# Kernel optimization log

Hardware: AMD Instinct MI355X
Metric: run time of the kernel (lower is better)

The kernel has to match this reference:

```python
import jax, jax.numpy as jnp
import numpy as np

B, L, D = 64, 512, 256
BT = 4            # behavior_types (== last dim of bs_seq)
USERS = 10000     # user_num
EPS = 1e-8


def _ln(x, w, b):
    u = x.mean(-1, keepdims=True)
    s = ((x - u) ** 2).mean(-1, keepdims=True)
    return w * (x - u) / jnp.sqrt(s + EPS) + b


def setup_inputs() -> dict:
    key = jax.random.key(0)
    ks = jax.random.split(key, 32)
    lin = lambda k: 0.02 * jax.random.normal(k, (D, D), dtype=jnp.float32)
    inp = {
        'u': jax.random.randint(ks[0], (B,), 0, USERS + 1),
        'seq_logits': jax.random.normal(ks[1], (B, L, D), dtype=jnp.float32),
        'item_emb': jax.random.normal(ks[2], (B, L, D), dtype=jnp.float32),
        'pos_emb': jax.random.normal(ks[3], (B, L, D), dtype=jnp.float32),
        'bs_seq': jax.random.randint(ks[4], (B, L, BT), 0, 2, dtype=jnp.int32),
        'bs_emb': jax.random.normal(ks[5], (B, L, D), dtype=jnp.float32),
        'attn_mask': jnp.zeros((B, 1, L, L), dtype=jnp.float32),
        'user_tables': 0.02 * jax.random.normal(ks[6], (USERS + 1, BT + 1), dtype=jnp.float32),
        'Wq_ib': lin(ks[7]), 'bq_ib': jnp.zeros(D),
        'Wk_ib': lin(ks[8]), 'bk_ib': jnp.zeros(D),
        'Wv_ib': lin(ks[9]), 'bv_ib': jnp.zeros(D),
        'Wq_pb': lin(ks[10]), 'bq_pb': jnp.zeros(D),
        'Wk_pb': lin(ks[11]), 'bk_pb': jnp.zeros(D),
        'Wv_pb': lin(ks[12]), 'bv_pb': jnp.zeros(D),
        'Wf': lin(ks[13]), 'bf': jnp.zeros(D),
        'ln_qib_w': jnp.ones(D), 'ln_qib_b': jnp.zeros(D),
        'ln_qpb_w': jnp.ones(D), 'ln_qpb_b': jnp.zeros(D),
        'ln_f_w': jnp.ones(D), 'ln_f_b': jnp.zeros(D),
    }
    return inp


def reference(u, seq_logits, item_emb, pos_emb, bs_seq, bs_emb, attn_mask,
              user_tables, Wq_ib, bq_ib, Wk_ib, bk_ib, Wv_ib, bv_ib,
              Wq_pb, bq_pb, Wk_pb, bk_pb, Wv_pb, bv_pb, Wf, bf,
              ln_qib_w, ln_qib_b, ln_qpb_w, ln_qpb_b, ln_f_w, ln_f_b):
    mask = attn_mask[:, 0]                      # (B, L, L)
    scale = 1.0 / jnp.sqrt(jnp.float32(D))

    # hamming-distance bias: pdist(hamming)*BT == integer mismatch count (bt==BT)
    dist_idx = jnp.sum(bs_seq[:, :, None, :] != bs_seq[:, None, :, :], axis=-1)  # (B,L,L) int
    tab = user_tables[u]                        # (B, BT+1) per-user transition table
    ham = jax.vmap(lambda t, idx: t[idx])(tab, dist_idx) * scale   # (B, L, L)
    ham_probs = jax.nn.softmax(ham + mask, axis=-1)

    def branch(x_in, ln_w, ln_b, Wq, bq, Wk, bk, Wv, bv):
        q = _ln(x_in, ln_w, ln_b) @ Wq + bq
        k = x_in @ Wk + bk
        v = x_in @ Wv + bv
        scores = jnp.einsum('bqd,bkd->bqk', q, k) * scale
        probs = jax.nn.softmax(scores + mask, axis=-1) + ham_probs
        return jnp.einsum('bqk,bkd->bqd', probs, v)

    ib = branch(item_emb + bs_emb, ln_qib_w, ln_qib_b, Wq_ib, bq_ib, Wk_ib, bk_ib, Wv_ib, bv_ib)
    pb = branch(pos_emb + bs_emb, ln_qpb_w, ln_qpb_b, Wq_pb, bq_pb, Wk_pb, bk_pb, Wv_pb, bv_pb)

    mha = (ib + pb) @ Wf + bf
    return _ln(mha + seq_logits + bs_emb, ln_f_w, ln_f_b)
```

## Files before the change

kernel.cpp:

```cpp
#include <hip/hip_runtime.h>
#include <hip/hip_bf16.h>
#include <math.h>

#define TB 256

typedef short bf16x8 __attribute__((ext_vector_type(8)));
typedef float f32x4 __attribute__((ext_vector_type(4)));
typedef unsigned short ushort_t;
typedef unsigned short us4 __attribute__((ext_vector_type(4)));
typedef unsigned short us8 __attribute__((ext_vector_type(8)));

constexpr int Bc = 64, Lc = 512, Dc = 256;
constexpr float kScale = 0.0625f;
constexpr float kEps = 1e-8f;

__device__ __forceinline__ ushort_t f2bf(float x) {
    union { float f; unsigned u; } v; v.f = x;
    unsigned r = v.u + 0x7fffu + ((v.u >> 16) & 1u);
    return (ushort_t)(r >> 16);
}
__device__ __forceinline__ float bf2f(ushort_t h) {
    union { float f; unsigned u; } v; v.u = ((unsigned)h) << 16;
    return v.f;
}
__device__ __forceinline__ void split1(float x, ushort_t& h, ushort_t& l) {
    h = f2bf(x);
    l = f2bf(x - bf2f(h));
}

__device__ __forceinline__ float sel5(float t0, float t1, float t2, float t3, float t4, int i) {
    float r = t0;
    r = (i == 1) ? t1 : r;
    r = (i == 2) ? t2 : r;
    r = (i == 3) ? t3 : r;
    r = (i == 4) ? t4 : r;
    return r;
}

__device__ __forceinline__ int swz(int row, int unit) {
    return row * 32 + ((unit ^ ((row >> 1) & 3)) << 3);
}

__global__ __launch_bounds__(TB) void tab_codes_kernel(
    const int* __restrict__ u, const float* __restrict__ user_tables,
    const int* __restrict__ bs_seq, int* __restrict__ codes, float* __restrict__ tabv)
{
    int gid = blockIdx.x * TB + threadIdx.x;
    const int R = Bc * Lc;
    if (gid < R) {
        const int* r = bs_seq + (size_t)gid * 4;
        int c = 0;
        #pragma unroll
        for (int t = 0; t < 4; ++t) c |= (r[t] != 0) << t;
        codes[gid] = c;
    }
    if (gid < Bc * 5) {
        int b = gid / 5, j = gid % 5;
        tabv[gid] = user_tables[(size_t)u[b] * 5 + j] * kScale;
    }
}

struct PtrSet { const float* src[7]; ushort_t* dstH[7]; ushort_t* dstL[7]; };

__global__ __launch_bounds__(TB) void wtrans_kernel(PtrSet ps)
{
    __shared__ alignas(16) float t[32][33];
    const float* S = ps.src[blockIdx.z];
    ushort_t* DH = ps.dstH[blockIdx.z];
    ushort_t* DL = ps.dstL[blockIdx.z];
    const int r0 = blockIdx.y * 32, c0 = blockIdx.x * 32;
    const int tx = threadIdx.x & 31, ty = threadIdx.x >> 5;
    #pragma unroll
    for (int i = 0; i < 32; i += 8) t[ty + i][tx] = S[(size_t)(r0 + ty + i) * Dc + c0 + tx];
    __syncthreads();
    #pragma unroll
    for (int i = 0; i < 32; i += 8) {
        float v = t[tx][ty + i];
        ushort_t h, l; split1(v, h, l);
        size_t o = (size_t)(c0 + ty + i) * Dc + r0 + tx;
        DH[o] = h; DL[o] = l;
    }
}

__global__ __launch_bounds__(TB) void prep_x_kernel(
    const float* __restrict__ a, const float* __restrict__ b,
    const float* __restrict__ lnw, const float* __restrict__ lnb,
    ushort_t* __restrict__ xh, ushort_t* __restrict__ xl,
    ushort_t* __restrict__ lh, ushort_t* __restrict__ ll)
{
    const int lane = threadIdx.x & 63;
    const int wv = threadIdx.x >> 6;
    const int row = blockIdx.x * 4 + wv;
    const int col = lane * 4;
    size_t base = (size_t)row * Dc + col;
    float4 av = *(const float4*)(a + base);
    float4 bv = *(const float4*)(b + base);
    float x4[4] = {av.x + bv.x, av.y + bv.y, av.z + bv.z, av.w + bv.w};
    float s = x4[0] + x4[1] + x4[2] + x4[3];
    float ss = x4[0]*x4[0] + x4[1]*x4[1] + x4[2]*x4[2] + x4[3]*x4[3];
    #pragma unroll
    for (int off = 32; off; off >>= 1) {
        s += __shfl_xor(s, off);
        ss += __shfl_xor(ss, off);
    }
    const float mu = s * (1.0f / Dc);
    const float var = ss * (1.0f / Dc) - mu * mu;
    const float rs = 1.0f / sqrtf(var + kEps);
    float4 w4 = *(const float4*)(lnw + col);
    float4 b4 = *(const float4*)(lnb + col);
    float wv_[4] = {w4.x, w4.y, w4.z, w4.w};
    float bb_[4] = {b4.x, b4.y, b4.z, b4.w};
    us4 XH, XL, LH, LL4;
    #pragma unroll
    for (int j = 0; j < 4; ++j) {
        ushort_t h, l;
        split1(x4[j], h, l); XH[j] = h; XL[j] = l;
        float ln = (x4[j] - mu) * rs * wv_[j] + bb_[j];
        split1(ln, h, l); LH[j] = h; LL4[j] = l;
    }
    *(us4*)(xh + base) = XH;
    *(us4*)(xl + base) = XL;
    *(us4*)(lh + base) = LH;
    *(us4*)(ll + base) = LL4;
}

template<int AMODE, int CMODE, bool BIAS, bool SCL, bool CADD>
__global__ __launch_bounds__(TB) void mfma_gemm(
    const ushort_t* __restrict__ aH, const ushort_t* __restrict__ aL,
    const float* __restrict__ a32,
    const ushort_t* __restrict__ bH, const ushort_t* __restrict__ bL,
    const float* __restrict__ bias,
    float* __restrict__ c32, ushort_t* __restrict__ cH, ushort_t* __restrict__ cL,
    int K, int lda, int ldb, int ldc,
    long sA, long sB, long sC, float scale)
{
    __shared__ alignas(16) ushort_t AsH[4096];
    __shared__ alignas(16) ushort_t AsL[4096];
    __shared__ alignas(16) ushort_t BsH[4096];
    __shared__ alignas(16) ushort_t BsL[4096];

    const int tid = threadIdx.x;
    const int bz = blockIdx.z;
    const int row0 = blockIdx.y * 128, col0 = blockIdx.x * 128;
    const int lane = tid & 63, wid = tid >> 6;
    const int wr = (wid >> 1) * 64, wc = (wid & 1) * 64;
    const int fr = lane & 15, fh = lane >> 4;
    const int su = tid & 3, sm = tid >> 2;

    const int dA0 = swz(sm, su), dA1 = swz(sm + 64, su);

    const ushort_t* aHp = nullptr; const ushort_t* aLp = nullptr;
    const float* a32p = nullptr;
    if constexpr (AMODE == 0) {
        aHp = aH + (size_t)bz * sA + (size_t)(row0 + sm) * lda + su * 8;
        aLp = aL + (size_t)bz * sA + (size_t)(row0 + sm) * lda + su * 8;
    } else {
        a32p = a32 + (size_t)bz * sA + (size_t)(row0 + sm) * lda + su * 8;
    }
    const ushort_t* bHp = bH + (size_t)bz * sB + (size_t)(col0 + sm) * ldb + su * 8;
    const ushort_t* bLp = bL + (size_t)bz * sB + (size_t)(col0 + sm) * ldb + su * 8;
    const size_t aHalf = (size_t)64 * lda;
    const size_t bHalf = (size_t)64 * ldb;

    int ai[4], bi[4];
    #pragma unroll
    for (int f = 0; f < 4; ++f) {
        ai[f] = swz(wr + f * 16 + fr, fh);
        bi[f] = swz(wc + f * 16 + fr, fh);
    }

    f32x4 acc[4][4] = {};

    for (int k0 = 0; k0 < K; k0 += 32) {
        if constexpr (AMODE == 0) {
            *(us8*)&AsH[dA0] = *(const us8*)(aHp + k0);
            *(us8*)&AsH[dA1] = *(const us8*)(aHp + aHalf + k0);
            *(us8*)&AsL[dA0] = *(const us8*)(aLp + k0);
            *(us8*)&AsL[dA1] = *(const us8*)(aLp + aHalf + k0);
        } else {
            #pragma unroll
            for (int half = 0; half < 2; ++half) {
                const size_t o = half * aHalf + k0;
                float v[8];
                *(float4*)&v[0] = *(const float4*)(a32p + o);
                *(float4*)&v[4] = *(const float4*)(a32p + o + 4);
                us8 h8, l8;
                #pragma unroll
                for (int j = 0; j < 8; ++j) {
                    ushort_t h, l; split1(v[j], h, l);
                    h8[j] = h; l8[j] = l;
                }
                const int di = half ? dA1 : dA0;
                *(us8*)&AsH[di] = h8;
                *(us8*)&AsL[di] = l8;
            }
        }
        *(us8*)&BsH[dA0] = *(const us8*)(bHp + k0);
        *(us8*)&BsH[dA1] = *(const us8*)(bHp + bHalf + k0);
        *(us8*)&BsL[dA0] = *(const us8*)(bLp + k0);
        *(us8*)&BsL[dA1] = *(const us8*)(bLp + bHalf + k0);
        __syncthreads();

        bf16x8 aHf[4], aLf[4], bHf[4], bLf[4];
        #pragma unroll
        for (int f = 0; f < 4; ++f) {
            aHf[f] = *(const bf16x8*)&AsH[ai[f]];
            aLf[f] = *(const bf16x8*)&AsL[ai[f]];
            bHf[f] = *(const bf16x8*)&BsH[bi[f]];
            bLf[f] = *(const bf16x8*)&BsL[bi[f]];
        }
        #pragma unroll
        for (int fj = 0; fj < 4; ++fj)
            #pragma unroll
            for (int fi = 0; fi < 4; ++fi)
                acc[fi][fj] = __builtin_amdgcn_mfma_f32_16x16x32_bf16(aHf[fi], bHf[fj], acc[fi][fj], 0, 0, 0);
        #pragma unroll
        for (int fj = 0; fj < 4; ++fj)
            #pragma unroll
            for (int fi = 0; fi < 4; ++fi)
                acc[fi][fj] = __builtin_amdgcn_mfma_f32_16x16x32_bf16(aHf[fi], bLf[fj], acc[fi][fj], 0, 0, 0);
        #pragma unroll
        for (int fj = 0; fj < 4; ++fj)
            #pragma unroll
            for (int fi = 0; fi < 4; ++fi)
                acc[fi][fj] = __builtin_amdgcn_mfma_f32_16x16x32_bf16(aLf[fi], bHf[fj], acc[fi][fj], 0, 0, 0);
        __syncthreads();
    }

    #pragma unroll
    for (int fj = 0; fj < 4; ++fj) {
        const int c = col0 + wc + fj * 16 + fr;
        const float bv = BIAS ? bias[c] : 0.0f;
        #pragma unroll
        for (int fi = 0; fi < 4; ++fi) {
            f32x4 a = acc[fi][fj];
            float o[4];
            #pragma unroll
            for (int j = 0; j < 4; ++j) o[j] = (SCL ? a[j] * scale : a[j]) + bv;
            const int r0 = row0 + wr + fi * 16 + fh * 4;
            if constexpr (CMODE == 0) {
                float* cp = c32 + (size_t)bz * sC + (size_t)r0 * ldc + c;
                #pragma unroll
                for (int j = 0; j < 4; ++j) {
                    if constexpr (CADD) cp[(size_t)j * ldc] += o[j];
                    else                cp[(size_t)j * ldc]  = o[j];
                }
            } else if constexpr (CMODE == 1) {
                #pragma unroll
                for (int j = 0; j < 4; ++j) {
                    ushort_t h, l; split1(o[j], h, l);
                    const size_t idx = (size_t)(r0 + j) * ldc + c;
                    cH[idx] = h; cL[idx] = l;
                }
            } else {
                us4 h4, l4;
                #pragma unroll
                for (int j = 0; j < 4; ++j) {
                    ushort_t h, l; split1(o[j], h, l);
                    h4[j] = h; l4[j] = l;
                }
                *(us4*)(cH + (size_t)c * ldc + r0) = h4;
                *(us4*)(cL + (size_t)c * ldc + r0) = l4;
            }
        }
    }
}

__global__ __launch_bounds__(TB) void softmax_ham_kernel(
    const float* __restrict__ S, const float* __restrict__ mask,
    const int* __restrict__ codes, const float* __restrict__ tabv,
    ushort_t* __restrict__ Ph, ushort_t* __restrict__ Pl)
{
    const int lane = threadIdx.x & 63;
    const int wv = threadIdx.x >> 6;
    const int row = blockIdx.x * 4 + wv;
    const int b = row >> 9;
    const float* srow = S + (size_t)row * Lc;
    const float* mrow = mask + (size_t)row * Lc;
    const int* crow = codes + (size_t)b * Lc;
    const int cq = codes[row];
    const float t0 = tabv[b * 5 + 0], t1 = tabv[b * 5 + 1], t2 = tabv[b * 5 + 2],
                t3 = tabv[b * 5 + 3], t4 = tabv[b * 5 + 4];
    float sv[8], hv[8];
    #pragma unroll
    for (int h = 0; h < 2; ++h) {
        int k = h * 256 + lane * 4;
        float4 s4 = *(const float4*)(srow + k);
        float4 m4 = *(const float4*)(mrow + k);
        int4 c4 = *(const int4*)(crow + k);
        sv[h * 4 + 0] = s4.x + m4.x;
        sv[h * 4 + 1] = s4.y + m4.y;
        sv[h * 4 + 2] = s4.z + m4.z;
        sv[h * 4 + 3] = s4.w + m4.w;
        hv[h * 4 + 0] = sel5(t0, t1, t2, t3, t4, __popc(cq ^ c4.x)) + m4.x;
        hv[h * 4 + 1] = sel5(t0, t1, t2, t3, t4, __popc(cq ^ c4.y)) + m4.y;
        hv[h * 4 + 2] = sel5(t0, t1, t2, t3, t4, __popc(cq ^ c4.z)) + m4.z;
        hv[h * 4 + 3] = sel5(t0, t1, t2, t3, t4, __popc(cq ^ c4.w)) + m4.w;
    }
    float m1 = -1e30f, m2 = -1e30f;
    #pragma unroll
    for (int i = 0; i < 8; ++i) { m1 = fmaxf(m1, sv[i]); m2 = fmaxf(m2, hv[i]); }
    #pragma unroll
    for (int off = 32; off; off >>= 1) {
        m1 = fmaxf(m1, __shfl_xor(m1, off));
        m2 = fmaxf(m2, __shfl_xor(m2, off));
    }
    float e1 = 0.f, e2 = 0.f;
    #pragma unroll
    for (int i = 0; i < 8; ++i) {
        sv[i] = expf(sv[i] - m1); e1 += sv[i];
        hv[i] = expf(hv[i] - m2); e2 += hv[i];
    }
    #pragma unroll
    for (int off = 32; off; off >>= 1) {
        e1 += __shfl_xor(e1, off);
        e2 += __shfl_xor(e2, off);
    }
    const float r1 = 1.0f / e1, r2 = 1.0f / e2;
    #pragma unroll
    for (int h = 0; h < 2; ++h) {
        int k = h * 256 + lane * 4;
        us4 h4, l4;
        #pragma unroll
        for (int j = 0; j < 4; ++j) {
            float p = sv[h * 4 + j] * r1 + hv[h * 4 + j] * r2;
            ushort_t hh, ll; split1(p, hh, ll);
            h4[j] = hh; l4[j] = ll;
        }
        *(us4*)(Ph + (size_t)row * Lc + k) = h4;
        *(us4*)(Pl + (size_t)row * Lc + k) = l4;
    }
}

__global__ __launch_bounds__(TB) void final_ln_kernel(
    const float* __restrict__ mha, const float* __restrict__ seq,
    const float* __restrict__ bs, const float* __restrict__ w,
    const float* __restrict__ bb, float* __restrict__ out)
{
    const int lane = threadIdx.x & 63;
    const int wv = threadIdx.x >> 6;
    const int row = blockIdx.x * 4 + wv;
    size_t base = (size_t)row * Dc + lane * 4;
    float4 a = *(const float4*)(mha + base);
    float4 b = *(const float4*)(seq + base);
    float4 c = *(const float4*)(bs + base);
    float4 t = make_float4(a.x + b.x + c.x, a.y + b.y + c.y, a.z + b.z + c.z, a.w + b.w + c.w);
    float s = t.x + t.y + t.z + t.w;
    float ss = t.x * t.x + t.y * t.y + t.z * t.z + t.w * t.w;
    #pragma unroll
    for (int off = 32; off; off >>= 1) {
        s += __shfl_xor(s, off);
        ss += __shfl_xor(ss, off);
    }
    float mu = s * (1.0f / Dc);
    float var = ss * (1.0f / Dc) - mu * mu;
    float rs = 1.0f / sqrtf(var + kEps);
    int col = lane * 4;
    float4 o;
    o.x = (t.x - mu) * rs * w[col + 0] + bb[col + 0];
    o.y = (t.y - mu) * rs * w[col + 1] + bb[col + 1];
    o.z = (t.z - mu) * rs * w[col + 2] + bb[col + 2];
    o.w = (t.w - mu) * rs * w[col + 3] + bb[col + 3];
    *(float4*)(out + base) = o;
}

extern "C" void kernel_launch(void* const* d_in, const int* in_sizes, int n_in,
                              void* d_out, int out_size, void* d_ws, size_t ws_size,
                              hipStream_t stream) {
    const int* u            = (const int*)d_in[0];
    const float* seq_logits = (const float*)d_in[1];
    const float* item_emb   = (const float*)d_in[2];
    const float* pos_emb    = (const float*)d_in[3];
    const int* bs_seq       = (const int*)d_in[4];
    const float* bs_emb     = (const float*)d_in[5];
    const float* attn_mask  = (const float*)d_in[6];
    const float* user_tab   = (const float*)d_in[7];
    const float* Wq_ib = (const float*)d_in[8];
    const float* bq_ib = (const float*)d_in[9];
    const float* Wk_ib = (const float*)d_in[10];
    const float* bk_ib = (const float*)d_in[11];
    const float* Wv_ib = (const float*)d_in[12];
    const float* bv_ib = (const float*)d_in[13];
    const float* Wq_pb = (const float*)d_in[14];
    const float* bq_pb = (const float*)d_in[15];
    const float* Wk_pb = (const float*)d_in[16];
    const float* bk_pb = (const float*)d_in[17];
    const float* Wv_pb = (const float*)d_in[18];
    const float* bv_pb = (const float*)d_in[19];
    const float* Wf    = (const float*)d_in[20];
    const float* bf    = (const float*)d_in[21];
    const float* ln_qib_w = (const float*)d_in[22];
    const float* ln_qib_b = (const float*)d_in[23];
    const float* ln_qpb_w = (const float*)d_in[24];
    const float* ln_qpb_b = (const float*)d_in[25];
    const float* ln_f_w   = (const float*)d_in[26];
    const float* ln_f_b   = (const float*)d_in[27];
    float* out = (float*)d_out;

    const size_t RD = (size_t)Bc * Lc * Dc;
    const size_t RL = (size_t)Bc * Lc * Lc;
    const size_t R  = (size_t)Bc * Lc;
    const size_t WSZ = (size_t)Dc * Dc;

    char* p = (char*)d_ws;
    ushort_t* xh   = (ushort_t*)p;
    ushort_t* xl   = xh + RD;
    ushort_t* lnh  = xl + RD;
    ushort_t* lnl  = lnh + RD;
    float*    Sb   = (float*)p;
    float*    x_mha= (float*)p;
    p += RL * 4;
    ushort_t* qh = (ushort_t*)p; ushort_t* ql = qh + RD; p += RD * 4;
    ushort_t* kh = (ushort_t*)p; ushort_t* kl = kh + RD; p += RD * 4;
    ushort_t* vTh = (ushort_t*)p; ushort_t* vTl = vTh + RD; p += RD * 4;
    float* O = (float*)p; p += RD * 4;
    ushort_t* WH[7]; ushort_t* WL[7];
    for (int i = 0; i < 7; ++i) {
        WH[i] = (ushort_t*)p; p += WSZ * 2;
        WL[i] = (ushort_t*)p; p += WSZ * 2;
    }
    float* tabv = (float*)p; p += 512 * 4;
    int* codes  = (int*)p;  p += R * 4;
    ushort_t* Ph = qh;
    ushort_t* Pl = kh;

    dim3 blk(TB);
    dim3 gRow((unsigned)(R / 4));
    dim3 gQKV(Dc / 128, (unsigned)(R / 128), 1);
    dim3 gS(Lc / 128, Lc / 128, Bc);
    dim3 gPV(Dc / 128, Lc / 128, Bc);
    const long LD = (long)Lc * Dc;
    const long LL = (long)Lc * Lc;

    tab_codes_kernel<<<dim3((unsigned)(R / TB)), blk, 0, stream>>>(u, user_tab, bs_seq, codes, tabv);

    PtrSet ps;
    const float* wsrc[7] = {Wq_ib, Wk_ib, Wv_ib, Wq_pb, Wk_pb, Wv_pb, Wf};
    for (int i = 0; i < 7; ++i) { ps.src[i] = wsrc[i]; ps.dstH[i] = WH[i]; ps.dstL[i] = WL[i]; }
    wtrans_kernel<<<dim3(8, 8, 7), blk, 0, stream>>>(ps);

    for (int br = 0; br < 2; ++br) {
        const float* emb = br == 0 ? item_emb : pos_emb;
        const ushort_t* WqH = WH[br * 3 + 0]; const ushort_t* WqL = WL[br * 3 + 0];
        const ushort_t* WkH = WH[br * 3 + 1]; const ushort_t* WkL = WL[br * 3 + 1];
        const ushort_t* WvH = WH[br * 3 + 2]; const ushort_t* WvL = WL[br * 3 + 2];
        const float* bq = br == 0 ? bq_ib : bq_pb;
        const float* bk = br == 0 ? bk_ib : bk_pb;
        const float* bv = br == 0 ? bv_ib : bv_pb;
        const float* lw = br == 0 ? ln_qib_w : ln_qpb_w;
        const float* lb = br == 0 ? ln_qib_b : ln_qpb_b;

        prep_x_kernel<<<gRow, blk, 0, stream>>>(emb, bs_emb, lw, lb, xh, xl, lnh, lnl);
        mfma_gemm<0, 1, true, false, false><<<gQKV, blk, 0, stream>>>(
            lnh, lnl, nullptr, WqH, WqL, bq, nullptr, qh, ql,
            Dc, Dc, Dc, Dc, 0, 0, 0, 1.0f);
        mfma_gemm<0, 1, true, false, false><<<gQKV, blk, 0, stream>>>(
            xh, xl, nullptr, WkH, WkL, bk, nullptr, kh, kl,
            Dc, Dc, Dc, Dc, 0, 0, 0, 1.0f);
        mfma_gemm<0, 2, true, false, false><<<gQKV, blk, 0, stream>>>(
            xh, xl, nullptr, WvH, WvL, bv, nullptr, vTh, vTl,
            Dc, Dc, Dc, (int)R, 0, 0, 0, 1.0f);
        mfma_gemm<0, 0, false, true, false><<<gS, blk, 0, stream>>>(
            qh, ql, nullptr, kh, kl, nullptr, Sb, nullptr, nullptr,
            Dc, Dc, Dc, Lc, LD, LD, LL, kScale);
        softmax_ham_kernel<<<gRow, blk, 0, stream>>>(Sb, attn_mask, codes, tabv, Ph, Pl);
        if (br == 0)
            mfma_gemm<0, 0, false, false, false><<<gPV, blk, 0, stream>>>(
                Ph, Pl, nullptr, vTh, vTl, nullptr, O, nullptr, nullptr,
                Lc, Lc, (int)R, Dc, LL, (long)Lc, LD, 1.0f);
        else
            mfma_gemm<0, 0, false, false, true><<<gPV, blk, 0, stream>>>(
                Ph, Pl, nullptr, vTh, vTl, nullptr, O, nullptr, nullptr,
                Lc, Lc, (int)R, Dc, LL, (long)Lc, LD, 1.0f);
    }

    mfma_gemm<1, 0, true, false, false><<<gQKV, blk, 0, stream>>>(
        nullptr, nullptr, O, WH[6], WL[6], bf, x_mha, nullptr, nullptr,
        Dc, Dc, Dc, Dc, 0, 0, 0, 1.0f);

    final_ln_kernel<<<gRow, blk, 0, stream>>>(x_mha, seq_logits, bs_emb, ln_f_w, ln_f_b, out);
}
```

Before: 762.2 us.

## Double-buffer B tiles via global_load_lds, load A directly, swizzle batched grids to XCDs

Restructures the split-bf16 MFMA GEMM. The B tile is double-buffered in LDS using async global_load_lds, so the next tile's load overlaps the current tile's MFMAs. A fragments are read straight from global memory into registers, with no LDS staging. Batched S and PV launches become 1D grids remapped so each batch stays on one XCD for L2 locality. V^T is now produced by swapping operands with a row bias rather than using a transposed-store epilogue. This risks uncoalesced per-lane global reads for A and a single barrier per iteration protecting the double buffer.

```diff
diff --git a/kernel.cpp b/kernel.cpp
--- a/kernel.cpp
+++ b/kernel.cpp
@@ -26,6 +26,12 @@
 __device__ __forceinline__ void split1(float x, ushort_t& h, ushort_t& l) {
     h = f2bf(x);
     l = f2bf(x - bf2f(h));
+}
+
+__device__ __forceinline__ void gl_lds16(const ushort_t* g, ushort_t* l) {
+    __builtin_amdgcn_global_load_lds(
+        (__attribute__((address_space(1))) void*)(g),
+        (__attribute__((address_space(3))) void*)(l), 16, 0, 0);
 }
 
 __device__ __forceinline__ float sel5(float t0, float t1, float t2, float t3, float t4, int i) {
@@ -124,7 +130,7 @@
     *(us4*)(ll + base) = LL4;
 }
 
-template<int AMODE, int CMODE, bool BIAS, bool SCL, bool CADD>
+template<int AMODE, int CMODE, int BIASN, bool SCL, bool CADD, bool XSWZ>
 __global__ __launch_bounds__(TB) void mfma_gemm(
     const ushort_t* __restrict__ aH, const ushort_t* __restrict__ aL,
     const float* __restrict__ a32,
@@ -132,82 +138,104 @@
     const float* __restrict__ bias,
     float* __restrict__ c32, ushort_t* __restrict__ cH, ushort_t* __restrict__ cL,
     int K, int lda, int ldb, int ldc,
-    long sA, long sB, long sC, float scale)
+    long sA, long sB, long sC, float scale,
+    int nxShift, int gShift)
 {
-    __shared__ alignas(16) ushort_t AsH[4096];
-    __shared__ alignas(16) ushort_t AsL[4096];
-    __shared__ alignas(16) ushort_t BsH[4096];
-    __shared__ alignas(16) ushort_t BsL[4096];
+    __shared__ alignas(16) ushort_t BsH[2][4096];
+    __shared__ alignas(16) ushort_t BsL[2][4096];
 
     const int tid = threadIdx.x;
-    const int bz = blockIdx.z;
-    const int row0 = blockIdx.y * 128, col0 = blockIdx.x * 128;
+    int bx, by, bz;
+    if constexpr (XSWZ) {
+        const int i = blockIdx.x;
+        const int xcd = i & 7;
+        const int slot = i >> 3;
+        const int tile = slot & ((1 << gShift) - 1);
+        bz = xcd + ((slot >> gShift) << 3);
+        bx = tile & ((1 << nxShift) - 1);
+        by = tile >> nxShift;
+    } else {
+        bx = blockIdx.x; by = blockIdx.y; bz = blockIdx.z;
+    }
+    const int row0 = by * 128, col0 = bx * 128;
     const int lane = tid & 63, wid = tid >> 6;
     const int wr = (wid >> 1) * 64, wc = (wid & 1) * 64;
     const int fr = lane & 15, fh = lane >> 4;
-    const int su = tid & 3, sm = tid >> 2;
-
-    const int dA0 = swz(sm, su), dA1 = swz(sm + 64, su);
-
-    const ushort_t* aHp = nullptr; const ushort_t* aLp = nullptr;
-    const float* a32p = nullptr;
-    if constexpr (AMODE == 0) {
-        aHp = aH + (size_t)bz * sA + (size_t)(row0 + sm) * lda + su * 8;
-        aLp = aL + (size_t)bz * sA + (size_t)(row0 + sm) * lda + su * 8;
-    } else {
-        a32p = a32 + (size_t)bz * sA + (size_t)(row0 + sm) * lda + su * 8;
-    }
-    const ushort_t* bHp = bH + (size_t)bz * sB + (size_t)(col0 + sm) * ldb + su * 8;
-    const ushort_t* bLp = bL + (size_t)bz * sB + (size_t)(col0 + sm) * ldb + su * 8;
-    const size_t aHalf = (size_t)64 * lda;
+
+    const int srow  = 16 * wid + (lane >> 2);
+    const int sunit = (lane & 3) ^ ((lane >> 3) & 3);
+    const ushort_t* bSrcH = bH + (size_t)bz * sB + (size_t)(col0 + srow) * ldb + sunit * 8;
+    const ushort_t* bSrcL = bL + (size_t)bz * sB + (size_t)(col0 + srow) * ldb + sunit * 8;
     const size_t bHalf = (size_t)64 * ldb;
-
-    int ai[4], bi[4];
+    const int ldsC = wid * 512;
+
+    int bi[4];
+    #pragma unroll
+    for (int f = 0; f < 4; ++f) bi[f] = swz(wc + f * 16 + fr, fh);
+
+    const ushort_t* aPH[4]; const ushort_t* aPL[4]; const float* aP32[4];
     #pragma unroll
     for (int f = 0; f < 4; ++f) {
-        ai[f] = swz(wr + f * 16 + fr, fh);
-        bi[f] = swz(wc + f * 16 + fr, fh);
+        const int r = row0 + wr + f * 16 + fr;
+        if constexpr (AMODE == 0) {
+            aPH[f] = aH + (size_t)bz * sA + (size_t)r * lda + fh * 8;
+            aPL[f] = aL + (size_t)bz * sA + (size_t)r * lda + fh * 8;
+        } else {
+            aP32[f] = a32 + (size_t)bz * sA + (size_t)r * lda + fh * 8;
+        }
     }
 
     f32x4 acc[4][4] = {};
-
-    for (int k0 = 0; k0 < K; k0 += 32) {
+    const int NT = K >> 5;
+
+    {
+        gl_lds16(bSrcH,         &BsH[0][ldsC]);
+        gl_lds16(bSrcH + bHalf, &BsH[0][2048 + ldsC]);
+        gl_lds16(bSrcL,         &BsL[0][ldsC]);
+        gl_lds16(bSrcL + bHalf, &BsL[0][2048 + ldsC]);
+    }
+
+    for (int t = 0; t < NT; ++t) {
+        __syncthreads();
+        if (t + 1 < NT) {
+            const int nb = (t + 1) & 1;
+            const ushort_t* hp = bSrcH + (size_t)(t + 1) * 32;
+            const ushort_t* lp = bSrcL + (size_t)(t + 1) * 32;
+            gl_lds16(hp,         &BsH[nb][ldsC]);
+            gl_lds16(hp + bHalf, &BsH[nb][2048 + ldsC]);
+            gl_lds16(lp,         &BsL[nb][ldsC]);
+            gl_lds16(lp + bHalf, &BsL[nb][2048 + ldsC]);
+        }
+        const int k0 = t * 32;
+        const int cb = t & 1;
+
+        bf16x8 aHf[4], aLf[4];
         if constexpr (AMODE == 0) {
-            *(us8*)&AsH[dA0] = *(const us8*)(aHp + k0);
-            *(us8*)&AsH[dA1] = *(const us8*)(aHp + aHalf + k0);
-            *(us8*)&AsL[dA0] = *(const us8*)(aLp + k0);
-            *(us8*)&AsL[dA1] = *(const us8*)(aLp + aHalf + k0);
+            #pragma unroll
+            for (int f = 0; f < 4; ++f) {
+                aHf[f] = *(const bf16x8*)(aPH[f] + k0);
+                aLf[f] = *(const bf16x8*)(aPL[f] + k0);
+            }
         } else {
             #pragma unroll
-            for (int half = 0; half < 2; ++half) {
-                const size_t o = half * aHalf + k0;
+            for (int f = 0; f < 4; ++f) {
                 float v[8];
-                *(float4*)&v[0] = *(const float4*)(a32p + o);
-                *(float4*)&v[4] = *(const float4*)(a32p + o + 4);
+                *(float4*)&v[0] = *(const float4*)(aP32[f] + k0);
+                *(float4*)&v[4] = *(const float4*)(aP32[f] + k0 + 4);
                 us8 h8, l8;
                 #pragma unroll
                 for (int j = 0; j < 8; ++j) {
                     ushort_t h, l; split1(v[j], h, l);
                     h8[j] = h; l8[j] = l;
                 }
-                const int di = half ? dA1 : dA0;
-                *(us8*)&AsH[di] = h8;
-                *(us8*)&AsL[di] = l8;
+                aHf[f] = (bf16x8)h8; aLf[f] = (bf16x8)l8;
             }
         }
-        *(us8*)&BsH[dA0] = *(const us8*)(bHp + k0);
-        *(us8*)&BsH[dA1] = *(const us8*)(bHp + bHalf + k0);
-        *(us8*)&BsL[dA0] = *(const us8*)(bLp + k0);
-        *(us8*)&BsL[dA1] = *(const us8*)(bLp + bHalf + k0);
-        __syncthreads();
-
-        bf16x8 aHf[4], aLf[4], bHf[4], bLf[4];
+        bf16x8 bHf[4], bLf[4];
         #pragma unroll
         for (int f = 0; f < 4; ++f) {
-            aHf[f] = *(const bf16x8*)&AsH[ai[f]];
-            aLf[f] = *(const bf16x8*)&AsL[ai[f]];
-            bHf[f] = *(const bf16x8*)&BsH[bi[f]];
-            bLf[f] = *(const bf16x8*)&BsL[bi[f]];
+            bHf[f] = *(const bf16x8*)&BsH[cb][bi[f]];
+            bLf[f] = *(const bf16x8*)&BsL[cb][bi[f]];
         }
         #pragma unroll
         for (int fj = 0; fj < 4; ++fj)
@@ -224,20 +252,24 @@
             #pragma unroll
             for (int fi = 0; fi < 4; ++fi)
                 acc[fi][fj] = __builtin_amdgcn_mfma_f32_16x16x32_bf16(aLf[fi], bHf[fj], acc[fi][fj], 0, 0, 0);
-        __syncthreads();
     }
 
     #pragma unroll
     for (int fj = 0; fj < 4; ++fj) {
         const int c = col0 + wc + fj * 16 + fr;
-        const float bv = BIAS ? bias[c] : 0.0f;
+        const float bcol = (BIASN == 1) ? bias[c] : 0.0f;
         #pragma unroll
         for (int fi = 0; fi < 4; ++fi) {
             f32x4 a = acc[fi][fj];
+            const int r0 = row0 + wr + fi * 16 + fh * 4;
             float o[4];
             #pragma unroll
-            for (int j = 0; j < 4; ++j) o[j] = (SCL ? a[j] * scale : a[j]) + bv;
-            const int r0 = row0 + wr + fi * 16 + fh * 4;
+            for (int j = 0; j < 4; ++j) {
+                float v = SCL ? a[j] * scale : a[j];
+                if constexpr (BIASN == 1) v += bcol;
+                if constexpr (BIASN == 2) v += bias[r0 + j];
+                o[j] = v;
+            }
             if constexpr (CMODE == 0) {
                 float* cp = c32 + (size_t)bz * sC + (size_t)r0 * ldc + c;
                 #pragma unroll
@@ -245,22 +277,13 @@
                     if constexpr (CADD) cp[(size_t)j * ldc] += o[j];
                     else                cp[(size_t)j * ldc]  = o[j];
                 }
-            } else if constexpr (CMODE == 1) {
+            } else {
                 #pragma unroll
                 for (int j = 0; j < 4; ++j) {
                     ushort_t h, l; split1(o[j], h, l);
                     const size_t idx = (size_t)(r0 + j) * ldc + c;
                     cH[idx] = h; cL[idx] = l;
                 }
-            } else {
-                us4 h4, l4;
-                #pragma unroll
-                for (int j = 0; j < 4; ++j) {
-                    ushort_t h, l; split1(o[j], h, l);
-                    h4[j] = h; l4[j] = l;
-                }
-                *(us4*)(cH + (size_t)c * ldc + r0) = h4;
-                *(us4*)(cL + (size_t)c * ldc + r0) = l4;
             }
         }
     }
@@ -427,8 +450,9 @@
     dim3 blk(TB);
     dim3 gRow((unsigned)(R / 4));
     dim3 gQKV(Dc / 128, (unsigned)(R / 128), 1);
-    dim3 gS(Lc / 128, Lc / 128, Bc);
-    dim3 gPV(Dc / 128, Lc / 128, Bc);
+    dim3 gVT((unsigned)(R / 128), Dc / 128, 1);
+    dim3 gS1(Bc * 16);
+    dim3 gPV1(Bc * 8);
     const long LD = (long)Lc * Dc;
     const long LL = (long)Lc * Lc;
 
@@ -451,32 +475,32 @@
         const float* lb = br == 0 ? ln_qib_b : ln_qpb_b;
 
         prep_x_kernel<<<gRow, blk, 0, stream>>>(emb, bs_emb, lw, lb, xh, xl, lnh, lnl);
-        mfma_gemm<0, 1, true, false, false><<<gQKV, blk, 0, stream>>>(
+        mfma_gemm<0, 1, 1, false, false, false><<<gQKV, blk, 0, stream>>>(
             lnh, lnl, nullptr, WqH, WqL, bq, nullptr, qh, ql,
-            Dc, Dc, Dc, Dc, 0, 0, 0, 1.0f);
-        mfma_gemm<0, 1, true, false, false><<<gQKV, blk, 0, stream>>>(
+            Dc, Dc, Dc, Dc, 0, 0, 0, 1.0f, 0, 0);
+        mfma_gemm<0, 1, 1, false, false, false><<<gQKV, blk, 0, stream>>>(
             xh, xl, nullptr, WkH, WkL, bk, nullptr, kh, kl,
-            Dc, Dc, Dc, Dc, 0, 0, 0, 1.0f);
-        mfma_gemm<0, 2, true, false, false><<<gQKV, blk, 0, stream>>>(
-            xh, xl, nullptr, WvH, WvL, bv, nullptr, vTh, vTl,
-            Dc, Dc, Dc, (int)R, 0, 0, 0, 1.0f);
-        mfma_gemm<0, 0, false, true, false><<<gS, blk, 0, stream>>>(
+            Dc, Dc, Dc, Dc, 0, 0, 0, 1.0f, 0, 0);
+        mfma_gemm<0, 1, 2, false, false, false><<<gVT, blk, 0, stream>>>(
+            WvH, WvL, nullptr, xh, xl, bv, nullptr, vTh, vTl,
+            Dc, Dc, Dc, (int)R, 0, 0, 0, 1.0f, 0, 0);
+        mfma_gemm<0, 0, 0, true, false, true><<<gS1, blk, 0, stream>>>(
             qh, ql, nullptr, kh, kl, nullptr, Sb, nullptr, nullptr,
-            Dc, Dc, Dc, Lc, LD, LD, LL, kScale);
+            Dc, Dc, Dc, Lc, LD, LD, LL, kScale, 2, 4);
         softmax_ham_kernel<<<gRow, blk, 0, stream>>>(Sb, attn_mask, codes, tabv, Ph, Pl);
         if (br == 0)
-            mfma_gemm<0, 0, false, false, false><<<gPV, blk, 0, stream>>>(
+            mfma_gemm<0, 0, 0, false, false, true><<<gPV1, blk, 0, stream>>>(
                 Ph, Pl, nullptr, vTh, vTl, nullptr, O, nullptr, nullptr,
-                Lc, Lc, (int)R, Dc, LL, (long)Lc, LD, 1.0f);
+                Lc, Lc, (int)R, Dc, LL, (long)Lc, LD, 1.0f, 1, 3);
         else
-            mfma_gemm<0, 0, false, false, true><<<gPV, blk, 0, stream>>>(
+            mfma_gemm<0, 0, 0, false, true, true><<<gPV1, blk, 0, stream>>>(
                 Ph, Pl, nullptr, vTh, vTl, nullptr, O, nullptr, nullptr,
-                Lc, Lc, (int)R, Dc, LL, (long)Lc, LD, 1.0f);
-    }
-
-    mfma_gemm<1, 0, true, false, false><<<gQKV, blk, 0, stream>>>(
+                Lc, Lc, (int)R, Dc, LL, (long)Lc, LD, 1.0f, 1, 3);
+    }
+
+    mfma_gemm<1, 0, 1, false, false, false><<<gQKV, blk, 0, stream>>>(
         nullptr, nullptr, O, WH[6], WL[6], bf, x_mha, nullptr, nullptr,
-        Dc, Dc, Dc, Dc, 0, 0, 0, 1.0f);
+        Dc, Dc, Dc, Dc, 0, 0, 0, 1.0f, 0, 0);
 
     final_ln_kernel<<<gRow, blk, 0, stream>>>(x_mha, seq_logits, bs_emb, ln_f_w, ln_f_b, out);
 }
```

After: 756.0 us. Within noise of the previous version (-0.8%).
